# Kernel optimization log

Measured on AMD Instinct MI355X. Metric: run time of the kernel, lower is better.

The kernel has to match this reference:

```python
import jax, jax.numpy as jnp
import numpy as np

N, D = 16384, 2048

def setup_inputs() -> dict:
    key = jax.random.key(0)
    k1, k2 = jax.random.split(key)
    F = jax.random.normal(k1, (N, D), dtype=jnp.float32)
    F_star = jax.random.normal(k2, (N, D), dtype=jnp.float32)
    lambda_r = jnp.float32(1.0)
    return {"F": F, "F_star": F_star, "lambda_r": lambda_r}

def reference(F, F_star, lambda_r):
    # trace(F F^T Fs Fs^T) == ||F^T Fs||_F^2 (cyclic trace property);
    # avoids materializing the n x n Gram matrices the torch code forms.
    G = jnp.einsum('nd,ne->de', F, F_star)  # [D, D]
    return lambda_r * jnp.sum(G * G)
```

## Files before the change

kernel.cpp:

```cpp
#include <hip/hip_runtime.h>
#include <hip/hip_bf16.h>

#define N_ROWS 16384
#define D_DIM  2048
#define SPLITK 4
#define NS     (N_ROWS / 32)
#define NP     (D_DIM / 128)


typedef __attribute__((ext_vector_type(8))) short short8;
typedef __attribute__((ext_vector_type(4))) float f32x4;
typedef __attribute__((ext_vector_type(8))) unsigned short ushort8;
typedef __attribute__((ext_vector_type(4))) unsigned short ushort4v;

#define GPTR(p) ((const __attribute__((address_space(1))) void*)(p))
#define LPTR(p) ((__attribute__((address_space(3))) void*)(p))

__device__ __forceinline__ unsigned short f2bf(float x) {
  __hip_bfloat16 b = __float2bfloat16(x);
  return *reinterpret_cast<unsigned short*>(&b);
}
__device__ __forceinline__ float bf2f(unsigned short u) {
  unsigned int v = ((unsigned int)u) << 16;
  return *reinterpret_cast<float*>(&v);
}

__global__ void __launch_bounds__(256) transpose_pack(
    const float* __restrict__ F, const float* __restrict__ Fs,
    unsigned short* __restrict__ Fb, unsigned short* __restrict__ Fsb) {
  const float* src = blockIdx.z ? Fs : F;
  unsigned short* dst = blockIdx.z ? Fsb : Fb;
  const int k0 = blockIdx.x * 128;
  const int mt = blockIdx.y;
  const int m0 = mt * 128;
  const int t = threadIdx.x;

  __shared__ unsigned short tile[128 * 136];
  unsigned int* tile32 = (unsigned int*)tile;

#pragma unroll
  for (int p = 0; p < 8; ++p) {
    const int id = p * 256 + t;
    const int mg = id & 31;
    const int kk = (id >> 5) * 2;
    const float4 r0 = *(const float4*)&src[(size_t)(k0 + kk) * D_DIM + m0 + mg * 4];
    const float4 r1 = *(const float4*)&src[(size_t)(k0 + kk + 1) * D_DIM + m0 + mg * 4];
    const float a0[4] = {r0.x, r0.y, r0.z, r0.w};
    const float a1[4] = {r1.x, r1.y, r1.z, r1.w};
#pragma unroll
    for (int mi = 0; mi < 4; ++mi) {
      const unsigned lo = f2bf(a0[mi]), hi = f2bf(a1[mi]);
      tile32[(mg * 4 + mi) * 68 + (kk >> 1)] = lo | (hi << 16);
    }
  }
  __syncthreads();

  const int w = t >> 6, lane = t & 63;
#pragma unroll
  for (int q = 0; q < 8; ++q) {
    const int ksl = q >> 1;
    const int tt = (q & 1) * 4 + w;
    const int m_l = tt * 16 + (lane & 15);
    const int k_l = ksl * 32 + (lane >> 4) * 8;
    const ushort8 v = *(const ushort8*)&tile[m_l * 136 + k_l];
    const size_t chunk = ((size_t)mt * NS + (k0 >> 5) + ksl) * 4096;
    *(ushort8*)&dst[chunk + (size_t)tt * 512 + lane * 8] = v;
  }
}

__global__ void __launch_bounds__(256) gemm_packed(
    const unsigned short* __restrict__ Fb, const unsigned short* __restrict__ Fsb,
    unsigned short* __restrict__ Cpart) {
  __shared__ unsigned short lds[8192];
  const int tid = threadIdx.x;
  const int wave = tid >> 6, lane = tid & 63;
  const int wm = wave >> 1, wn = wave & 1;
  const int z = blockIdx.z;
  const int NSs = NS / SPLITK;

  size_t offA = ((size_t)blockIdx.y * NS + (size_t)z * NSs) * 4096 + (size_t)(2 * wave) * 512 + lane * 8;
  size_t offB = ((size_t)blockIdx.x * NS + (size_t)z * NSs) * 4096 + (size_t)(2 * wave) * 512 + lane * 8;
  unsigned short* lA = &lds[(2 * wave) * 512];
  unsigned short* lB = &lds[4096 + (2 * wave) * 512];

  f32x4 acc[4][4];
#pragma unroll
  for (int i = 0; i < 4; ++i)
#pragma unroll
    for (int j = 0; j < 4; ++j) acc[i][j] = 0.f;

  const unsigned short* lfa = &lds[(wm * 4) * 512];
  const unsigned short* lfb = &lds[4096 + (wn * 4) * 512];

  for (int it = 0; it < NSs; ++it) {
    __builtin_amdgcn_global_load_lds(GPTR(Fb + offA), LPTR(lA), 16, 0, 0);
    __builtin_amdgcn_global_load_lds(GPTR(Fb + offA + 512), LPTR(lA + 512), 16, 0, 0);
    __builtin_amdgcn_global_load_lds(GPTR(Fsb + offB), LPTR(lB), 16, 0, 0);
    __builtin_amdgcn_global_load_lds(GPTR(Fsb + offB + 512), LPTR(lB + 512), 16, 0, 0);
    offA += 4096; offB += 4096;
    __syncthreads();

    short8 a[4], b[4];
#pragma unroll
    for (int i = 0; i < 4; ++i) a[i] = *(const short8*)&lfa[i * 512 + lane * 8];
#pragma unroll
    for (int j = 0; j < 4; ++j) b[j] = *(const short8*)&lfb[j * 512 + lane * 8];
#pragma unroll
    for (int i = 0; i < 4; ++i)
#pragma unroll
      for (int j = 0; j < 4; ++j)
        acc[i][j] = __builtin_amdgcn_mfma_f32_16x16x32_bf16(a[i], b[j], acc[i][j], 0, 0, 0);
    __syncthreads();
  }

  unsigned short* cp = Cpart + (size_t)z * (D_DIM * D_DIM)
                     + (size_t)(blockIdx.y * 16 + blockIdx.x) * 16384 + wave * 4096;
#pragma unroll
  for (int i = 0; i < 4; ++i)
#pragma unroll
    for (int j = 0; j < 4; ++j) {
      ushort4v o;
#pragma unroll
      for (int r = 0; r < 4; ++r) o[r] = f2bf(acc[i][j][r]);
      *(ushort4v*)&cp[(i * 4 + j) * 256 + lane * 4] = o;
    }
}

__global__ void __launch_bounds__(256) reduce_squares(
    const unsigned short* __restrict__ Cpart, const float* __restrict__ lam,
    float* __restrict__ out) {
  const int NQ = (D_DIM * D_DIM) / 8;
  const ushort8* c = (const ushort8*)Cpart;
  float s = 0.f;
  for (int idx = blockIdx.x * 256 + threadIdx.x; idx < NQ; idx += gridDim.x * 256) {
    float v[8];
#pragma unroll
    for (int j = 0; j < 8; ++j) v[j] = 0.f;
#pragma unroll
    for (int z = 0; z < SPLITK; ++z) {
      ushort8 u = c[(size_t)z * NQ + idx];
#pragma unroll
      for (int j = 0; j < 8; ++j) v[j] += bf2f(u[j]);
    }
#pragma unroll
    for (int j = 0; j < 8; ++j) s += v[j] * v[j];
  }
  for (int off = 32; off > 0; off >>= 1) s += __shfl_down(s, off, 64);
  __shared__ float red[4];
  const int wave = threadIdx.x >> 6, lane = threadIdx.x & 63;
  if (lane == 0) red[wave] = s;
  __syncthreads();
  if (threadIdx.x == 0) atomicAdd(out, (red[0] + red[1] + red[2] + red[3]) * lam[0]);
}

__global__ void __launch_bounds__(256) fallback_kernel(
    const float* __restrict__ F, const float* __restrict__ Fs,
    const float* __restrict__ lam, float* __restrict__ out) {
  __shared__ float sA[64][16], sB[64][16];
  const int d0 = blockIdx.y * 16, e0 = blockIdx.x * 16;
  const int t = threadIdx.x;
  const int td = t >> 4, te = t & 15;
  float s = 0.f;
  for (int k0 = 0; k0 < N_ROWS; k0 += 64) {
#pragma unroll
    for (int p = 0; p < 4; ++p) {
      const int k = (t >> 4) + p * 16;
      const int cc = t & 15;
      sA[k][cc] = F[(size_t)(k0 + k) * D_DIM + d0 + cc];
      sB[k][cc] = Fs[(size_t)(k0 + k) * D_DIM + e0 + cc];
    }
    __syncthreads();
#pragma unroll
    for (int kk = 0; kk < 64; ++kk) s += sA[kk][td] * sB[kk][te];
    __syncthreads();
  }
  float q = s * s;
  for (int off = 32; off > 0; off >>= 1) q += __shfl_down(q, off, 64);
  __shared__ float red[4];
  if ((t & 63) == 0) red[t >> 6] = q;
  __syncthreads();
  if (t == 0) atomicAdd(out, (red[0] + red[1] + red[2] + red[3]) * lam[0]);
}

extern "C" void kernel_launch(void* const* d_in, const int* in_sizes, int n_in,
                              void* d_out, int out_size, void* d_ws, size_t ws_size,
                              hipStream_t stream) {
  const float* F   = (const float*)d_in[0];
  const float* Fs  = (const float*)d_in[1];
  const float* lam = (const float*)d_in[2];
  float* out = (float*)d_out;
  hipMemsetAsync(d_out, 0, sizeof(float) * (size_t)out_size, stream);

  const size_t bf_bytes = (size_t)NP * NS * 8192;
  const size_t cpart_bytes = (size_t)SPLITK * D_DIM * D_DIM * 2;
  const size_t need = 2 * bf_bytes + cpart_bytes;

  if (ws_size >= need) {
    unsigned short* Fb  = (unsigned short*)d_ws;
    unsigned short* Fsb = Fb + bf_bytes / 2;
    unsigned short* Cpart = (unsigned short*)((char*)d_ws + 2 * bf_bytes);
    transpose_pack<<<dim3(128, 16, 2), 256, 0, stream>>>(F, Fs, Fb, Fsb);
    gemm_packed<<<dim3(16, 16, SPLITK), 256, 0, stream>>>(Fb, Fsb, Cpart);
    reduce_squares<<<dim3(1024), 256, 0, stream>>>(Cpart, lam, out);
  } else {
    fallback_kernel<<<dim3(128, 128), 256, 0, stream>>>(F, Fs, lam, out);
  }
}
```

Before: 508.1 us.

## Register-transpose pack without LDS and double K-slab per GEMM iteration

The transpose/pack kernel now has each thread load eight rows into registers and write packed bf16 chunks directly, dropping the LDS tile and its barrier and using 64-row blocks (twice as many blocks). The GEMM loads two 32-wide K slabs per iteration into a doubled LDS buffer, halving the number of barrier pairs per MFMA. The costs are more registers in the pack kernel, potentially less coalesced 16-byte stores, and double the LDS footprint in the GEMM, which may lower occupancy.

```diff
diff --git a/kernel.cpp b/kernel.cpp
--- a/kernel.cpp
+++ b/kernel.cpp
@@ -30,58 +30,52 @@
     unsigned short* __restrict__ Fb, unsigned short* __restrict__ Fsb) {
   const float* src = blockIdx.z ? Fs : F;
   unsigned short* dst = blockIdx.z ? Fsb : Fb;
-  const int k0 = blockIdx.x * 128;
+  const int t = threadIdx.x;
   const int mt = blockIdx.y;
   const int m0 = mt * 128;
-  const int t = threadIdx.x;
-
-  __shared__ unsigned short tile[128 * 136];
-  unsigned int* tile32 = (unsigned int*)tile;
-
-#pragma unroll
-  for (int p = 0; p < 8; ++p) {
-    const int id = p * 256 + t;
-    const int mg = id & 31;
-    const int kk = (id >> 5) * 2;
-    const float4 r0 = *(const float4*)&src[(size_t)(k0 + kk) * D_DIM + m0 + mg * 4];
-    const float4 r1 = *(const float4*)&src[(size_t)(k0 + kk + 1) * D_DIM + m0 + mg * 4];
-    const float a0[4] = {r0.x, r0.y, r0.z, r0.w};
-    const float a1[4] = {r1.x, r1.y, r1.z, r1.w};
-#pragma unroll
-    for (int mi = 0; mi < 4; ++mi) {
-      const unsigned lo = f2bf(a0[mi]), hi = f2bf(a1[mi]);
-      tile32[(mg * 4 + mi) * 68 + (kk >> 1)] = lo | (hi << 16);
-    }
-  }
-  __syncthreads();
-
-  const int w = t >> 6, lane = t & 63;
-#pragma unroll
-  for (int q = 0; q < 8; ++q) {
-    const int ksl = q >> 1;
-    const int tt = (q & 1) * 4 + w;
-    const int m_l = tt * 16 + (lane & 15);
-    const int k_l = ksl * 32 + (lane >> 4) * 8;
-    const ushort8 v = *(const ushort8*)&tile[m_l * 136 + k_l];
-    const size_t chunk = ((size_t)mt * NS + (k0 >> 5) + ksl) * 4096;
-    *(ushort8*)&dst[chunk + (size_t)tt * 512 + lane * 8] = v;
+  const int kb0 = blockIdx.x * 64;
+
+  const int mg   = t & 31;
+  const int koct = (t >> 5) & 3;
+  const int c    = t >> 7;
+  const int krow = kb0 + c * 32 + koct * 8;
+
+  float4 r[8];
+#pragma unroll
+  for (int j = 0; j < 8; ++j)
+    r[j] = *(const float4*)&src[(size_t)(krow + j) * D_DIM + m0 + mg * 4];
+  const float* rp = (const float*)r;
+
+  const int ks = blockIdx.x * 2 + c;
+  unsigned short* base = dst + ((size_t)mt * NS + ks) * 4096
+                       + (size_t)(mg >> 2) * 512 + (size_t)koct * 128
+                       + (size_t)(mg & 3) * 32;
+#pragma unroll
+  for (int i = 0; i < 4; ++i) {
+    ushort8 o;
+#pragma unroll
+    for (int j = 0; j < 8; ++j) o[j] = f2bf(rp[j * 4 + i]);
+    *(ushort8*)&base[i * 8] = o;
   }
 }
 
 __global__ void __launch_bounds__(256) gemm_packed(
     const unsigned short* __restrict__ Fb, const unsigned short* __restrict__ Fsb,
     unsigned short* __restrict__ Cpart) {
-  __shared__ unsigned short lds[8192];
+  __shared__ unsigned short lds[16384];
   const int tid = threadIdx.x;
   const int wave = tid >> 6, lane = tid & 63;
   const int wm = wave >> 1, wn = wave & 1;
   const int z = blockIdx.z;
   const int NSs = NS / SPLITK;
-
-  size_t offA = ((size_t)blockIdx.y * NS + (size_t)z * NSs) * 4096 + (size_t)(2 * wave) * 512 + lane * 8;
-  size_t offB = ((size_t)blockIdx.x * NS + (size_t)z * NSs) * 4096 + (size_t)(2 * wave) * 512 + lane * 8;
+  const int NIT = NSs / 2;
+
+  size_t offA = ((size_t)blockIdx.y * NS + (size_t)z * NSs) * 4096
+              + (size_t)(2 * wave) * 512 + lane * 8;
+  size_t offB = ((size_t)blockIdx.x * NS + (size_t)z * NSs) * 4096
+              + (size_t)(2 * wave) * 512 + lane * 8;
   unsigned short* lA = &lds[(2 * wave) * 512];
-  unsigned short* lB = &lds[4096 + (2 * wave) * 512];
+  unsigned short* lB = &lds[8192 + (2 * wave) * 512];
 
   f32x4 acc[4][4];
 #pragma unroll
@@ -89,27 +83,33 @@
 #pragma unroll
     for (int j = 0; j < 4; ++j) acc[i][j] = 0.f;
 
-  const unsigned short* lfa = &lds[(wm * 4) * 512];
-  const unsigned short* lfb = &lds[4096 + (wn * 4) * 512];
-
-  for (int it = 0; it < NSs; ++it) {
-    __builtin_amdgcn_global_load_lds(GPTR(Fb + offA), LPTR(lA), 16, 0, 0);
-    __builtin_amdgcn_global_load_lds(GPTR(Fb + offA + 512), LPTR(lA + 512), 16, 0, 0);
-    __builtin_amdgcn_global_load_lds(GPTR(Fsb + offB), LPTR(lB), 16, 0, 0);
-    __builtin_amdgcn_global_load_lds(GPTR(Fsb + offB + 512), LPTR(lB + 512), 16, 0, 0);
-    offA += 4096; offB += 4096;
-    __syncthreads();
-
-    short8 a[4], b[4];
-#pragma unroll
-    for (int i = 0; i < 4; ++i) a[i] = *(const short8*)&lfa[i * 512 + lane * 8];
-#pragma unroll
-    for (int j = 0; j < 4; ++j) b[j] = *(const short8*)&lfb[j * 512 + lane * 8];
-#pragma unroll
-    for (int i = 0; i < 4; ++i)
+  for (int it = 0; it < NIT; ++it) {
+    __builtin_amdgcn_global_load_lds(GPTR(Fb + offA),              LPTR(lA),              16, 0, 0);
+    __builtin_amdgcn_global_load_lds(GPTR(Fb + offA + 512),        LPTR(lA + 512),        16, 0, 0);
+    __builtin_amdgcn_global_load_lds(GPTR(Fb + offA + 4096),       LPTR(lA + 4096),       16, 0, 0);
+    __builtin_amdgcn_global_load_lds(GPTR(Fb + offA + 4096 + 512), LPTR(lA + 4096 + 512), 16, 0, 0);
+    __builtin_amdgcn_global_load_lds(GPTR(Fsb + offB),              LPTR(lB),              16, 0, 0);
+    __builtin_amdgcn_global_load_lds(GPTR(Fsb + offB + 512),        LPTR(lB + 512),        16, 0, 0);
+    __builtin_amdgcn_global_load_lds(GPTR(Fsb + offB + 4096),       LPTR(lB + 4096),       16, 0, 0);
+    __builtin_amdgcn_global_load_lds(GPTR(Fsb + offB + 4096 + 512), LPTR(lB + 4096 + 512), 16, 0, 0);
+    offA += 8192; offB += 8192;
+    __syncthreads();
+
+#pragma unroll
+    for (int s = 0; s < 2; ++s) {
+      short8 a[4], b[4];
+#pragma unroll
+      for (int i = 0; i < 4; ++i)
+        a[i] = *(const short8*)&lds[s * 4096 + (wm * 4 + i) * 512 + lane * 8];
 #pragma unroll
       for (int j = 0; j < 4; ++j)
-        acc[i][j] = __builtin_amdgcn_mfma_f32_16x16x32_bf16(a[i], b[j], acc[i][j], 0, 0, 0);
+        b[j] = *(const short8*)&lds[8192 + s * 4096 + (wn * 4 + j) * 512 + lane * 8];
+#pragma unroll
+      for (int i = 0; i < 4; ++i)
+#pragma unroll
+        for (int j = 0; j < 4; ++j)
+          acc[i][j] = __builtin_amdgcn_mfma_f32_16x16x32_bf16(a[i], b[j], acc[i][j], 0, 0, 0);
+    }
     __syncthreads();
   }
 
@@ -199,7 +199,7 @@
     unsigned short* Fb  = (unsigned short*)d_ws;
     unsigned short* Fsb = Fb + bf_bytes / 2;
     unsigned short* Cpart = (unsigned short*)((char*)d_ws + 2 * bf_bytes);
-    transpose_pack<<<dim3(128, 16, 2), 256, 0, stream>>>(F, Fs, Fb, Fsb);
+    transpose_pack<<<dim3(N_ROWS / 64, NP, 2), 256, 0, stream>>>(F, Fs, Fb, Fsb);
     gemm_packed<<<dim3(16, 16, SPLITK), 256, 0, stream>>>(Fb, Fsb, Cpart);
     reduce_squares<<<dim3(1024), 256, 0, stream>>>(Cpart, lam, out);
   } else {
```

Result: no change. 501.9 us (-1.2%).
